# Kernel optimization log

Measured on AMD Instinct MI355X. Metric: run time of the kernel, lower is better.

Reference implementation:

```python
import jax, jax.numpy as jnp
import numpy as np

WS = (7, 7)          # window size
DIM = 256            # projection_dim
HEADS = 8
B = 2048             # batch * num_windows
NW = 64              # windows per image (mask leading dim)


def _relative_position_index(ws):
    coords = np.stack(np.meshgrid(np.arange(ws[0]), np.arange(ws[1]), indexing='ij'))  # [2,h,w]
    flat = coords.reshape(2, -1)                                   # [2, h*w]
    rel = flat[:, :, None] - flat[:, None, :]                      # [2, N, N]
    rel = rel.transpose(1, 2, 0)                                   # [N, N, 2]
    rel[:, :, 0] += ws[0] - 1
    rel[:, :, 1] += ws[1] - 1
    idx = rel[:, :, 0] * (2 * ws[1] - 1) + rel[:, :, 1]            # [N, N]
    return idx.reshape(-1).astype(np.int32)                        # [N*N]


def setup_inputs() -> dict:
    key = jax.random.key(0)
    ks = jax.random.split(key, 6)
    N = WS[0] * WS[1]
    return {
        'x': jax.random.normal(ks[0], (B, N, DIM), jnp.float32),
        'mask': jax.random.normal(ks[1], (NW, N, N), jnp.float32),  # additive shift mask
        'qkv_w': jax.random.normal(ks[2], (DIM, 3 * DIM), jnp.float32) * (DIM ** -0.5),
        'qkv_b': jnp.zeros((3 * DIM,), jnp.float32),
        'proj_w': jax.random.normal(ks[3], (DIM, DIM), jnp.float32) * (DIM ** -0.5),
        'proj_b': jnp.zeros((DIM,), jnp.float32),
        'bias_table': jax.random.normal(ks[4], ((2 * WS[0] - 1) * (2 * WS[1] - 1), HEADS), jnp.float32) * 0.02,
        'rel_index': jnp.asarray(_relative_position_index(WS)),
    }


def reference(x, mask, qkv_w, qkv_b, proj_w, proj_b, bias_table, rel_index):
    Bn, N, C = x.shape
    hd = C // HEADS
    scale = hd ** -0.5
    qkv = x @ qkv_w + qkv_b                               # [B, N, 3C]
    qkv = qkv.reshape(Bn, N, 3, HEADS, hd).transpose(2, 0, 3, 1, 4)  # [3, B, H, N, hd]
    q, k, v = qkv[0], qkv[1], qkv[2]
    attn = jnp.einsum('bhnd,bhmd->bhnm', q * scale, k)    # [B, H, N, N]
    # gathered relative position bias: [N*N, H] -> [H, N, N]
    bias = bias_table[rel_index].reshape(N, N, HEADS).transpose(2, 0, 1)
    attn = attn + bias[None]
    nW = mask.shape[0]
    attn = attn.reshape(Bn // nW, nW, HEADS, N, N) + mask[None, :, None]
    attn = attn.reshape(Bn, HEADS, N, N)
    attn = jax.nn.softmax(attn, axis=-1)
    out = jnp.einsum('bhnm,bhmd->bhnd', attn, v)          # [B, H, N, hd]
    out = out.transpose(0, 2, 1, 3).reshape(Bn, N, C)
    return out @ proj_w + proj_b
```

## Files before the change

### kernel.cpp

```cpp
#include <hip/hip_runtime.h>


typedef __attribute__((ext_vector_type(8))) short v8s;
typedef __attribute__((ext_vector_type(4))) float v4f;

__device__ __forceinline__ unsigned short f2bf(float f) {
    union { float f; unsigned int i; } v; v.f = f;
    unsigned int x = v.i;
    return (unsigned short)((x + 0x7fffu + ((x >> 16) & 1u)) >> 16);
}

#define NW1 196608
#define NW2 65536
#define NB1 768
#define NCB 1605632
#define QSCALE_LOG2E 0.25503487f
#define LOG2E 1.4426950408889634f

__global__ void wattn_preproc(const float* __restrict__ qkv_w,
                              const float* __restrict__ qkv_b,
                              const float* __restrict__ proj_w,
                              const float* __restrict__ bias_table,
                              const float* __restrict__ mask,
                              const int* __restrict__ rel_index,
                              unsigned short* __restrict__ W1f,
                              unsigned short* __restrict__ W2f,
                              float* __restrict__ B1v,
                              float* __restrict__ CBf)
{
    const int idx = blockIdx.x * 256 + threadIdx.x;
    if (idx < NW1) {
        const int j = idx & 7, l = (idx >> 3) & 63, s = (idx >> 9) & 7, T = idx >> 12;
        const int k = s * 32 + (l >> 4) * 8 + j;
        const int n = T * 16 + (l & 15);
        const int hh = n / 96, sub = n % 96;
        const int col = (sub < 32) ? (hh * 32 + sub)
                      : (sub < 64) ? (256 + hh * 32 + (sub - 32))
                                   : (512 + hh * 32 + (sub - 64));
        float v = qkv_w[k * 768 + col];
        if (sub < 32) v *= QSCALE_LOG2E;
        W1f[idx] = f2bf(v);
    } else if (idx < NW1 + NW2) {
        const int t = idx - NW1;
        const int j = t & 7, l = (t >> 3) & 63, s = (t >> 9) & 7, T = t >> 12;
        const int k = s * 32 + (l >> 4) * 8 + j;
        const int n = T * 16 + (l & 15);
        W2f[t] = f2bf(proj_w[k * 256 + n]);
    } else if (idx < NW1 + NW2 + NB1) {
        const int n = idx - NW1 - NW2;
        const int hh = n / 96, sub = n % 96;
        const int col = (sub < 32) ? (hh * 32 + sub)
                      : (sub < 64) ? (256 + hh * 32 + (sub - 32))
                                   : (512 + hh * 32 + (sub - 64));
        float v = qkv_b[col];
        if (sub < 32) v *= QSCALE_LOG2E;
        B1v[n] = v;
    } else {
        const int t = idx - (NW1 + NW2 + NB1);
        if (t < NCB) {
            const int c = t & 63;
            const int rr = t >> 6;
            const int r = rr % 49;
            const int q2 = rr / 49;
            const int hh = q2 & 7;
            const int w = q2 >> 3;
            float v;
            if (c < 49) {
                const int ri = rel_index[r * 49 + c];
                v = (bias_table[ri * 8 + hh] + mask[(w * 49 + r) * 49 + c]) * LOG2E;
            } else {
                v = -1e30f;
            }
            CBf[t] = v;
        }
    }
}

__global__ __launch_bounds__(256, 2)
void wattn_main(const float* __restrict__ x,
                const unsigned short* __restrict__ W1f,
                const float* __restrict__ B1v,
                const float* __restrict__ CB,
                const unsigned short* __restrict__ W2f,
                const float* __restrict__ proj_b,
                float* __restrict__ out)
{
    __shared__ __align__(16) unsigned short xs[49 * 72];
    __shared__ __align__(16) unsigned short wreg[4][5832];
    __shared__ __align__(16) unsigned short Os[49 * 264];

    const int tid  = threadIdx.x;
    const int wave = tid >> 6;
    const int lane = tid & 63;
    const int quad = lane >> 4;
    const int l15  = lane & 15;
    const int b    = blockIdx.x;
    const int widx = b & 63;
    const float* xw = x + (long)b * 49 * 256;
    const v4f zero4 = {0.0f, 0.0f, 0.0f, 0.0f};
    unsigned short* Wr = wreg[wave];

    int arow[4];
    #pragma unroll
    for (int mt = 0; mt < 4; ++mt) {
        int m = mt * 16 + l15; if (m > 48) m = 48;
        arow[mt] = m * 72 + quad * 8;
    }

    #pragma unroll 1
    for (int p = 0; p < 2; ++p) {
        v4f acc[6][4];
        #pragma unroll
        for (int i = 0; i < 6; ++i)
            #pragma unroll
            for (int mt = 0; mt < 4; ++mt) acc[i][mt] = zero4;

        const int T0 = p * 24 + wave * 6;
        const unsigned short* bb = W1f + T0 * 4096 + lane * 8;

        #pragma unroll 1
        for (int ch = 0; ch < 4; ++ch) {
            __syncthreads();
            for (int i = tid; i < 784; i += 256) {
                const int r = i >> 4, cq = i & 15;
                const float4 v = *reinterpret_cast<const float4*>(xw + r * 256 + ch * 64 + cq * 4);
                ushort4 o;
                o.x = f2bf(v.x); o.y = f2bf(v.y); o.z = f2bf(v.z); o.w = f2bf(v.w);
                *reinterpret_cast<ushort4*>(&xs[r * 72 + cq * 4]) = o;
            }
            __syncthreads();
            #pragma unroll
            for (int s = 0; s < 2; ++s) {
                v8s afr[4];
                #pragma unroll
                for (int mt = 0; mt < 4; ++mt)
                    afr[mt] = *reinterpret_cast<const v8s*>(&xs[arow[mt] + s * 32]);
                v8s bfr[6];
                #pragma unroll
                for (int i = 0; i < 6; ++i)
                    bfr[i] = *reinterpret_cast<const v8s*>(bb + i * 4096 + (ch * 2 + s) * 512);
                #pragma unroll
                for (int i = 0; i < 6; ++i)
                    #pragma unroll
                    for (int mt = 0; mt < 4; ++mt)
                        acc[i][mt] = __builtin_amdgcn_mfma_f32_16x16x32_bf16(afr[mt], bfr[i], acc[i][mt], 0, 0, 0);
            }
        }
        #pragma unroll
        for (int i = 0; i < 6; ++i) {
            const float bv = B1v[(T0 + i) * 16 + l15];
            #pragma unroll
            for (int mt = 0; mt < 4; ++mt) {
                acc[i][mt].x += bv; acc[i][mt].y += bv; acc[i][mt].z += bv; acc[i][mt].w += bv;
            }
        }

        const int h = p * 4 + wave;

        #pragma unroll
        for (int i = 0; i < 4; ++i) {
            const int base = (i < 2) ? 0 : 1960;
            const int c = (i & 1) * 16 + l15;
            #pragma unroll
            for (int mt = 0; mt < 4; ++mt) {
                const int m0 = mt * 16 + quad * 4;
                #pragma unroll
                for (int r = 0; r < 4; ++r)
                    if (m0 + r < 49) Wr[base + (m0 + r) * 40 + c] = f2bf(acc[i][mt][r]);
            }
        }

        v8s aq[4], bk[4];
        #pragma unroll
        for (int t = 0; t < 4; ++t) {
            int rq = t * 16 + l15; if (rq > 48) rq = 48;
            aq[t] = *reinterpret_cast<const v8s*>(&Wr[rq * 40 + quad * 8]);
            bk[t] = *reinterpret_cast<const v8s*>(&Wr[1960 + rq * 40 + quad * 8]);
        }
        v4f sacc[4][4];
        #pragma unroll
        for (int mt = 0; mt < 4; ++mt)
            #pragma unroll
            for (int nt = 0; nt < 4; ++nt)
                sacc[mt][nt] = __builtin_amdgcn_mfma_f32_16x16x32_bf16(aq[mt], bk[nt], zero4, 0, 0, 0);

        const float* cbb = CB + ((long)widx * 8 + h) * 49 * 64;
        #pragma unroll
        for (int mt = 0; mt < 4; ++mt) {
            float pout[4][4];
            #pragma unroll
            for (int r = 0; r < 4; ++r) {
                const int m = mt * 16 + quad * 4 + r;
                const int mc = m > 48 ? 48 : m;
                float s0 = sacc[mt][0][r] + cbb[mc * 64 + l15];
                float s1 = sacc[mt][1][r] + cbb[mc * 64 + 16 + l15];
                float s2 = sacc[mt][2][r] + cbb[mc * 64 + 32 + l15];
                float s3 = sacc[mt][3][r] + cbb[mc * 64 + 48 + l15];
                float mx = fmaxf(fmaxf(s0, s1), fmaxf(s2, s3));
                #pragma unroll
                for (int off = 1; off < 16; off <<= 1) mx = fmaxf(mx, __shfl_xor(mx, off, 16));
                const float e0 = __builtin_exp2f(s0 - mx);
                const float e1 = __builtin_exp2f(s1 - mx);
                const float e2 = __builtin_exp2f(s2 - mx);
                const float e3 = __builtin_exp2f(s3 - mx);
                float sm = (e0 + e1) + (e2 + e3);
                #pragma unroll
                for (int off = 1; off < 16; off <<= 1) sm += __shfl_xor(sm, off, 16);
                const float rs = __builtin_amdgcn_rcpf(sm);
                pout[r][0] = e0 * rs; pout[r][1] = e1 * rs;
                pout[r][2] = e2 * rs; pout[r][3] = e3 * rs;
            }
            #pragma unroll
            for (int r = 0; r < 4; ++r) {
                const int m = mt * 16 + quad * 4 + r;
                if (m < 49) {
                    #pragma unroll
                    for (int nt = 0; nt < 4; ++nt)
                        Wr[m * 72 + nt * 16 + l15] = f2bf(pout[r][nt]);
                }
            }
        }

        #pragma unroll
        for (int i = 4; i < 6; ++i) {
            const int d = (i - 4) * 16 + l15;
            #pragma unroll
            for (int mt = 0; mt < 4; ++mt) {
                const int m0 = mt * 16 + quad * 4;
                if (mt < 3) {
                    ushort4 pk;
                    pk.x = f2bf(acc[i][mt][0]); pk.y = f2bf(acc[i][mt][1]);
                    pk.z = f2bf(acc[i][mt][2]); pk.w = f2bf(acc[i][mt][3]);
                    *reinterpret_cast<ushort4*>(&Wr[3528 + d * 72 + m0]) = pk;
                } else if (quad == 0) {
                    Wr[3528 + d * 72 + 48] = f2bf(acc[i][mt][0]);
                }
            }
        }
        {
            const int d  = lane >> 1;
            const int c0 = 49 + (lane & 1) * 8;
            const int ce = (lane & 1) ? 64 : 57;
            for (int c = c0; c < ce; ++c) Wr[3528 + d * 72 + c] = 0;
        }

        v8s bv2[2][2];
        #pragma unroll
        for (int n2 = 0; n2 < 2; ++n2)
            #pragma unroll
            for (int kt = 0; kt < 2; ++kt)
                bv2[n2][kt] = *reinterpret_cast<const v8s*>(&Wr[3528 + (n2 * 16 + l15) * 72 + kt * 32 + quad * 8]);
        #pragma unroll
        for (int mt = 0; mt < 4; ++mt) {
            int mrc = mt * 16 + l15; if (mrc > 48) mrc = 48;
            v4f oacc[2] = {zero4, zero4};
            #pragma unroll
            for (int kt = 0; kt < 2; ++kt) {
                const v8s ap = *reinterpret_cast<const v8s*>(&Wr[mrc * 72 + kt * 32 + quad * 8]);
                #pragma unroll
                for (int n2 = 0; n2 < 2; ++n2)
                    oacc[n2] = __builtin_amdgcn_mfma_f32_16x16x32_bf16(ap, bv2[n2][kt], oacc[n2], 0, 0, 0);
            }
            #pragma unroll
            for (int n2 = 0; n2 < 2; ++n2) {
                const int c = h * 32 + n2 * 16 + l15;
                #pragma unroll
                for (int r = 0; r < 4; ++r) {
                    const int m = mt * 16 + quad * 4 + r;
                    if (m < 49) Os[m * 264 + c] = f2bf(oacc[n2][r]);
                }
            }
        }
    }

    __syncthreads();

    v4f pacc[4][4];
    #pragma unroll
    for (int i = 0; i < 4; ++i)
        #pragma unroll
        for (int mt = 0; mt < 4; ++mt) pacc[i][mt] = zero4;

    int orow[4];
    #pragma unroll
    for (int mt = 0; mt < 4; ++mt) {
        int m = mt * 16 + l15; if (m > 48) m = 48;
        orow[mt] = m * 264 + quad * 8;
    }
    const unsigned short* wb = W2f + (wave * 4) * 4096 + lane * 8;

    #pragma unroll
    for (int s = 0; s < 8; ++s) {
        v8s afr[4];
        #pragma unroll
        for (int mt = 0; mt < 4; ++mt)
            afr[mt] = *reinterpret_cast<const v8s*>(&Os[orow[mt] + s * 32]);
        #pragma unroll
        for (int i = 0; i < 4; ++i) {
            const v8s bfp = *reinterpret_cast<const v8s*>(wb + i * 4096 + s * 512);
            #pragma unroll
            for (int mt = 0; mt < 4; ++mt)
                pacc[i][mt] = __builtin_amdgcn_mfma_f32_16x16x32_bf16(afr[mt], bfp, pacc[i][mt], 0, 0, 0);
        }
    }

    #pragma unroll
    for (int i = 0; i < 4; ++i) {
        const int c = (wave * 4 + i) * 16 + l15;
        const float pb = proj_b[c];
        #pragma unroll
        for (int mt = 0; mt < 4; ++mt) {
            #pragma unroll
            for (int r = 0; r < 4; ++r) {
                const int m = mt * 16 + quad * 4 + r;
                if (m < 49) out[((long)b * 49 + m) * 256 + c] = pacc[i][mt][r] + pb;
            }
        }
    }
}

extern "C" void kernel_launch(void* const* d_in, const int* in_sizes, int n_in,
                              void* d_out, int out_size, void* d_ws, size_t ws_size,
                              hipStream_t stream)
{
    const float* x          = (const float*)d_in[0];
    const float* mask       = (const float*)d_in[1];
    const float* qkv_w      = (const float*)d_in[2];
    const float* qkv_b      = (const float*)d_in[3];
    const float* proj_w     = (const float*)d_in[4];
    const float* proj_b     = (const float*)d_in[5];
    const float* bias_table = (const float*)d_in[6];
    const int*   rel_index  = (const int*)d_in[7];
    float* out = (float*)d_out;

    char* ws = (char*)d_ws;
    unsigned short* W1f = (unsigned short*)(ws);
    unsigned short* W2f = (unsigned short*)(ws + 393216);
    float*          B1v = (float*)(ws + 524288);
    float*          CBf = (float*)(ws + 527360);

    wattn_preproc<<<7299, 256, 0, stream>>>(qkv_w, qkv_b, proj_w, bias_table, mask,
                                            rel_index, W1f, W2f, B1v, CBf);
    wattn_main<<<2048, 256, 0, stream>>>(x, W1f, B1v, CBf, W2f, proj_b, out);
}
```

Baseline: 350.0 us.

## Shrink shared memory, build V fragments via shuffles, permute bias layout

Cuts per-wave LDS regions by aliasing the x staging buffer onto the wave scratch, narrowing the Q/K row stride, and no longer staging V in LDS. The V B-operands are built directly from packed accumulators with cross-lane shuffles. The combined bias/mask table is permuted so each lane reads one float4, and the x staging chunk is widened to 128 columns so there are fewer barriers. Together these aim for 3 blocks per CU instead of 2. The price is an extra barrier, more shuffle instructions, more register pressure under the tighter launch bounds, and possible LDS bank conflicts from the 36-element stride.

```diff
diff --git a/kernel.cpp b/kernel.cpp
--- a/kernel.cpp
+++ b/kernel.cpp
@@ -2,12 +2,16 @@
 
 
 typedef __attribute__((ext_vector_type(8))) short v8s;
+typedef __attribute__((ext_vector_type(4))) short v4s;
 typedef __attribute__((ext_vector_type(4))) float v4f;
 
 __device__ __forceinline__ unsigned short f2bf(float f) {
     union { float f; unsigned int i; } v; v.f = f;
     unsigned int x = v.i;
     return (unsigned short)((x + 0x7fffu + ((x >> 16) & 1u)) >> 16);
+}
+__device__ __forceinline__ unsigned int pk2bf(float a, float b) {
+    return (unsigned int)f2bf(a) | ((unsigned int)f2bf(b) << 16);
 }
 
 #define NW1 196608
@@ -64,10 +68,11 @@
             const int q2 = rr / 49;
             const int hh = q2 & 7;
             const int w = q2 >> 3;
+            const int c_old = ((c & 3) << 4) | (c >> 2);
             float v;
-            if (c < 49) {
-                const int ri = rel_index[r * 49 + c];
-                v = (bias_table[ri * 8 + hh] + mask[(w * 49 + r) * 49 + c]) * LOG2E;
+            if (c_old < 49) {
+                const int ri = rel_index[r * 49 + c_old];
+                v = (bias_table[ri * 8 + hh] + mask[(w * 49 + r) * 49 + c_old]) * LOG2E;
             } else {
                 v = -1e30f;
             }
@@ -76,7 +81,7 @@
     }
 }
 
-__global__ __launch_bounds__(256, 2)
+__global__ __launch_bounds__(256, 3)
 void wattn_main(const float* __restrict__ x,
                 const unsigned short* __restrict__ W1f,
                 const float* __restrict__ B1v,
@@ -85,9 +90,9 @@
                 const float* __restrict__ proj_b,
                 float* __restrict__ out)
 {
-    __shared__ __align__(16) unsigned short xs[49 * 72];
-    __shared__ __align__(16) unsigned short wreg[4][5832];
+    __shared__ __align__(16) unsigned short wreg[4 * 3528];
     __shared__ __align__(16) unsigned short Os[49 * 264];
+    unsigned short* const xs = wreg;
 
     const int tid  = threadIdx.x;
     const int wave = tid >> 6;
@@ -98,13 +103,13 @@
     const int widx = b & 63;
     const float* xw = x + (long)b * 49 * 256;
     const v4f zero4 = {0.0f, 0.0f, 0.0f, 0.0f};
-    unsigned short* Wr = wreg[wave];
+    unsigned short* const Wr = wreg + wave * 3528;
 
     int arow[4];
     #pragma unroll
     for (int mt = 0; mt < 4; ++mt) {
         int m = mt * 16 + l15; if (m > 48) m = 48;
-        arow[mt] = m * 72 + quad * 8;
+        arow[mt] = m * 136 + quad * 8;
     }
 
     #pragma unroll 1
@@ -119,18 +124,18 @@
         const unsigned short* bb = W1f + T0 * 4096 + lane * 8;
 
         #pragma unroll 1
-        for (int ch = 0; ch < 4; ++ch) {
+        for (int ch = 0; ch < 2; ++ch) {
             __syncthreads();
-            for (int i = tid; i < 784; i += 256) {
-                const int r = i >> 4, cq = i & 15;
-                const float4 v = *reinterpret_cast<const float4*>(xw + r * 256 + ch * 64 + cq * 4);
+            for (int i = tid; i < 1568; i += 256) {
+                const int r = i >> 5, cq = i & 31;
+                const float4 v = *reinterpret_cast<const float4*>(xw + r * 256 + ch * 128 + cq * 4);
                 ushort4 o;
                 o.x = f2bf(v.x); o.y = f2bf(v.y); o.z = f2bf(v.z); o.w = f2bf(v.w);
-                *reinterpret_cast<ushort4*>(&xs[r * 72 + cq * 4]) = o;
+                *reinterpret_cast<ushort4*>(&xs[r * 136 + cq * 4]) = o;
             }
             __syncthreads();
             #pragma unroll
-            for (int s = 0; s < 2; ++s) {
+            for (int s = 0; s < 4; ++s) {
                 v8s afr[4];
                 #pragma unroll
                 for (int mt = 0; mt < 4; ++mt)
@@ -138,7 +143,7 @@
                 v8s bfr[6];
                 #pragma unroll
                 for (int i = 0; i < 6; ++i)
-                    bfr[i] = *reinterpret_cast<const v8s*>(bb + i * 4096 + (ch * 2 + s) * 512);
+                    bfr[i] = *reinterpret_cast<const v8s*>(bb + i * 4096 + (ch * 4 + s) * 512);
                 #pragma unroll
                 for (int i = 0; i < 6; ++i)
                     #pragma unroll
@@ -155,18 +160,29 @@
             }
         }
 
+        unsigned int vpk[2][4][2];
+        #pragma unroll
+        for (int iv = 0; iv < 2; ++iv)
+            #pragma unroll
+            for (int mt = 0; mt < 4; ++mt) {
+                vpk[iv][mt][0] = pk2bf(acc[4 + iv][mt][0], acc[4 + iv][mt][1]);
+                vpk[iv][mt][1] = pk2bf(acc[4 + iv][mt][2], acc[4 + iv][mt][3]);
+            }
+
+        __syncthreads();
+
         const int h = p * 4 + wave;
 
         #pragma unroll
         for (int i = 0; i < 4; ++i) {
-            const int base = (i < 2) ? 0 : 1960;
+            const int base = (i < 2) ? 0 : 1764;
             const int c = (i & 1) * 16 + l15;
             #pragma unroll
             for (int mt = 0; mt < 4; ++mt) {
                 const int m0 = mt * 16 + quad * 4;
                 #pragma unroll
                 for (int r = 0; r < 4; ++r)
-                    if (m0 + r < 49) Wr[base + (m0 + r) * 40 + c] = f2bf(acc[i][mt][r]);
+                    if (m0 + r < 49) Wr[base + (m0 + r) * 36 + c] = f2bf(acc[i][mt][r]);
             }
         }
 
@@ -174,8 +190,13 @@
         #pragma unroll
         for (int t = 0; t < 4; ++t) {
             int rq = t * 16 + l15; if (rq > 48) rq = 48;
-            aq[t] = *reinterpret_cast<const v8s*>(&Wr[rq * 40 + quad * 8]);
-            bk[t] = *reinterpret_cast<const v8s*>(&Wr[1960 + rq * 40 + quad * 8]);
+            const int qo = rq * 36 + quad * 8;
+            const v4s qlo = *reinterpret_cast<const v4s*>(&Wr[qo]);
+            const v4s qhi = *reinterpret_cast<const v4s*>(&Wr[qo + 4]);
+            aq[t] = __builtin_shufflevector(qlo, qhi, 0, 1, 2, 3, 4, 5, 6, 7);
+            const v4s klo = *reinterpret_cast<const v4s*>(&Wr[1764 + qo]);
+            const v4s khi = *reinterpret_cast<const v4s*>(&Wr[1764 + qo + 4]);
+            bk[t] = __builtin_shufflevector(klo, khi, 0, 1, 2, 3, 4, 5, 6, 7);
         }
         v4f sacc[4][4];
         #pragma unroll
@@ -187,15 +208,15 @@
         const float* cbb = CB + ((long)widx * 8 + h) * 49 * 64;
         #pragma unroll
         for (int mt = 0; mt < 4; ++mt) {
-            float pout[4][4];
             #pragma unroll
             for (int r = 0; r < 4; ++r) {
                 const int m = mt * 16 + quad * 4 + r;
                 const int mc = m > 48 ? 48 : m;
-                float s0 = sacc[mt][0][r] + cbb[mc * 64 + l15];
-                float s1 = sacc[mt][1][r] + cbb[mc * 64 + 16 + l15];
-                float s2 = sacc[mt][2][r] + cbb[mc * 64 + 32 + l15];
-                float s3 = sacc[mt][3][r] + cbb[mc * 64 + 48 + l15];
+                const float4 cb4 = *reinterpret_cast<const float4*>(cbb + mc * 64 + l15 * 4);
+                float s0 = sacc[mt][0][r] + cb4.x;
+                float s1 = sacc[mt][1][r] + cb4.y;
+                float s2 = sacc[mt][2][r] + cb4.z;
+                float s3 = sacc[mt][3][r] + cb4.w;
                 float mx = fmaxf(fmaxf(s0, s1), fmaxf(s2, s3));
                 #pragma unroll
                 for (int off = 1; off < 16; off <<= 1) mx = fmaxf(mx, __shfl_xor(mx, off, 16));
@@ -207,49 +228,35 @@
                 #pragma unroll
                 for (int off = 1; off < 16; off <<= 1) sm += __shfl_xor(sm, off, 16);
                 const float rs = __builtin_amdgcn_rcpf(sm);
-                pout[r][0] = e0 * rs; pout[r][1] = e1 * rs;
-                pout[r][2] = e2 * rs; pout[r][3] = e3 * rs;
-            }
-            #pragma unroll
-            for (int r = 0; r < 4; ++r) {
-                const int m = mt * 16 + quad * 4 + r;
                 if (m < 49) {
-                    #pragma unroll
-                    for (int nt = 0; nt < 4; ++nt)
-                        Wr[m * 72 + nt * 16 + l15] = f2bf(pout[r][nt]);
+                    Wr[m * 72 + l15]      = f2bf(e0 * rs);
+                    Wr[m * 72 + 16 + l15] = f2bf(e1 * rs);
+                    Wr[m * 72 + 32 + l15] = f2bf(e2 * rs);
+                    Wr[m * 72 + 48 + l15] = f2bf(e3 * rs);
                 }
             }
         }
 
-        #pragma unroll
-        for (int i = 4; i < 6; ++i) {
-            const int d = (i - 4) * 16 + l15;
-            #pragma unroll
-            for (int mt = 0; mt < 4; ++mt) {
-                const int m0 = mt * 16 + quad * 4;
-                if (mt < 3) {
-                    ushort4 pk;
-                    pk.x = f2bf(acc[i][mt][0]); pk.y = f2bf(acc[i][mt][1]);
-                    pk.z = f2bf(acc[i][mt][2]); pk.w = f2bf(acc[i][mt][3]);
-                    *reinterpret_cast<ushort4*>(&Wr[3528 + d * 72 + m0]) = pk;
-                } else if (quad == 0) {
-                    Wr[3528 + d * 72 + 48] = f2bf(acc[i][mt][0]);
+        const int srcA = ((quad & 1) << 5) + l15;
+        v8s bvf[2][2];
+        #pragma unroll
+        for (int kt = 0; kt < 2; ++kt) {
+            #pragma unroll
+            for (int iv = 0; iv < 2; ++iv) {
+                union { unsigned int u[4]; v8s v; } bw;
+                #pragma unroll
+                for (int hw = 0; hw < 2; ++hw) {
+                    const unsigned int aA = (unsigned int)__shfl((int)vpk[iv][2 * kt][hw],     srcA);
+                    const unsigned int bA = (unsigned int)__shfl((int)vpk[iv][2 * kt + 1][hw], srcA);
+                    bw.u[hw] = (quad & 2) ? bA : aA;
+                    const unsigned int aB = (unsigned int)__shfl((int)vpk[iv][2 * kt][hw],     srcA + 16);
+                    const unsigned int bB = (unsigned int)__shfl((int)vpk[iv][2 * kt + 1][hw], srcA + 16);
+                    bw.u[2 + hw] = (quad & 2) ? bB : aB;
                 }
-            }
-        }
-        {
-            const int d  = lane >> 1;
-            const int c0 = 49 + (lane & 1) * 8;
-            const int ce = (lane & 1) ? 64 : 57;
-            for (int c = c0; c < ce; ++c) Wr[3528 + d * 72 + c] = 0;
-        }
-
-        v8s bv2[2][2];
-        #pragma unroll
-        for (int n2 = 0; n2 < 2; ++n2)
-            #pragma unroll
-            for (int kt = 0; kt < 2; ++kt)
-                bv2[n2][kt] = *reinterpret_cast<const v8s*>(&Wr[3528 + (n2 * 16 + l15) * 72 + kt * 32 + quad * 8]);
+                bvf[kt][iv] = bw.v;
+            }
+        }
+
         #pragma unroll
         for (int mt = 0; mt < 4; ++mt) {
             int mrc = mt * 16 + l15; if (mrc > 48) mrc = 48;
@@ -257,9 +264,8 @@
             #pragma unroll
             for (int kt = 0; kt < 2; ++kt) {
                 const v8s ap = *reinterpret_cast<const v8s*>(&Wr[mrc * 72 + kt * 32 + quad * 8]);
-                #pragma unroll
-                for (int n2 = 0; n2 < 2; ++n2)
-                    oacc[n2] = __builtin_amdgcn_mfma_f32_16x16x32_bf16(ap, bv2[n2][kt], oacc[n2], 0, 0, 0);
+                oacc[0] = __builtin_amdgcn_mfma_f32_16x16x32_bf16(ap, bvf[kt][0], oacc[0], 0, 0, 0);
+                oacc[1] = __builtin_amdgcn_mfma_f32_16x16x32_bf16(ap, bvf[kt][1], oacc[1], 0, 0, 0);
             }
             #pragma unroll
             for (int n2 = 0; n2 < 2; ++n2) {
```

Result: slower. 546.9 us (+56.3%).
